# Kernel tuning notes

Measured on AMD Instinct MI355X. Metric: run time of the kernel, lower is better.

The kernel has to match this reference:

```python
import jax, jax.numpy as jnp
import numpy as np

WINDOW = 64
BAND_NUM = 2 * WINDOW      # 128
FILTER_LEN = 6 * WINDOW    # 384


def setup_inputs() -> dict:
    key = jax.random.key(0)
    k1, k2 = jax.random.split(key)
    B, C, T, F = 16, 1, 8192, WINDOW + 1  # F = band_num/2 + 1 = 65
    inp = jax.random.normal(k1, (B, C, T, F), dtype=jnp.float32)
    subband_filter = jax.random.normal(k2, (FILTER_LEN,), dtype=jnp.float32)
    lengths = jnp.full((B,), T, dtype=jnp.int32)  # one sample per batch element, all length T
    return {"input": inp, "subband_filter": subband_filter, "lengths": lengths}


def reference(input, subband_filter, lengths):
    B, C, T, F = input.shape
    S = lengths.shape[0]               # sample_num (static)
    x = input.reshape(-1, F)           # (N, F), N = B*C*T
    # torch.fft.irfft(norm='forward') -> jnp.fft.irfft(norm='forward'), out len = 2*(F-1) = band_num
    ifft_out = jnp.fft.irfft(x, norm='forward')          # (N, 128)
    # tile across the 3 band repeats, apply prototype filter and window gain
    wide = jnp.concatenate([ifft_out, ifft_out, ifft_out], axis=1)  # (N, 384)
    wide = wide * subband_filter[None, :] * WINDOW
    N = wide.shape[0]
    H = N // S                          # in_height (= C*T per sample)
    w = wide.reshape(S, H, 6, WINDOW)   # per-sample, per-frame, 6 taps of width `window`
    true_len = H - 5
    # overlap-add: out[s, t] = sum_k w[s, t + 5 - k, k]
    out = w[:, 5:H, 0, :]
    for k in range(1, 6):
        out = out + w[:, 5 - k:H - k, k, :]
    out = out.reshape(B, C, -1)         # (B, C, true_len*window)
    return out / 32768.0
```

## Files before the change

### kernel.cpp

```cpp
#include <hip/hip_runtime.h>
#include <hip/hip_bf16.h>


#define NF 65
#define NT 8192
#define TRUE_LEN 8187
#define FPW 59
#define WPB 139
#define TAB_STRIDE 68
#define YS_STRIDE 66

typedef const __attribute__((address_space(4))) float cfloat;

__device__ float d_tab[33 * TAB_STRIDE];

__global__ void build_tab_kernel() {
    int idx = blockIdx.x * 256 + threadIdx.x;
    if (idx >= 33 * TAB_STRIDE) return;
    int p = idx / TAB_STRIDE, n = idx % TAB_STRIDE;
    if (n >= 65) { d_tab[idx] = 0.0f; return; }
    int m = (n < 33) ? 2 * n : 2 * (n - 33) + 1;
    float w = (m == 0 || m == 64) ? 1.0f : 2.0f;
    int a = (m * p) & 127;
    d_tab[idx] = w * cospif((float)a * (1.0f / 64.0f));
}

__global__ __launch_bounds__(256)
void subband_main_kernel(const float* __restrict__ g_in,
                         const float* __restrict__ g_filt,
                         float* __restrict__ g_out)
{
    __shared__ __hip_bfloat16 Ys[4][64 * YS_STRIDE];

    const int tid  = threadIdx.x;
    const int lane = tid & 63;
    const int wv   = tid >> 6;
    const int wg   = blockIdx.x * 4 + wv;
    const int s     = wg / WPB;
    const int fbase = (wg % WPB) * FPW;
    int h = fbase + lane;
    if (h > NT - 1) h = NT - 1;

    const float* xr = g_in + ((size_t)s * NT + h) * NF;
    float X[NF];
    #pragma unroll
    for (int c = 0; c < 16; ++c) {
        float t4[4];
        __builtin_memcpy(t4, xr + 4 * c, 16);
        X[4 * c + 0] = t4[0]; X[4 * c + 1] = t4[1];
        X[4 * c + 2] = t4[2]; X[4 * c + 3] = t4[3];
    }
    X[64] = xr[64];

    __hip_bfloat16* ys = &Ys[wv][0];
    cfloat* ct = (cfloat*)(unsigned long long)(const float*)d_tab;

    for (int p = 0; p < 33; ++p) {
        cfloat* cf = ct + p * TAB_STRIDE;
        float e0 = 0.0f, e1 = 0.0f, o0 = 0.0f, o1 = 0.0f;
        #pragma unroll
        for (int n = 0; n < 32; n += 2) {
            e0 += cf[n]      * X[2 * n];
            e1 += cf[n + 1]  * X[2 * n + 2];
            o0 += cf[33 + n] * X[2 * n + 1];
            o1 += cf[34 + n] * X[2 * n + 3];
        }
        e0 += cf[32] * X[64];
        const float aE = e0 + e1, aO = o0 + o1;
        ys[lane * YS_STRIDE + p]      = __float2bfloat16(aE + aO);
        ys[lane * YS_STRIDE + 64 - p] = __float2bfloat16(aE - aO);
    }

    const int j = lane;
    float fc[6];
    #pragma unroll
    for (int k = 0; k < 6; ++k) fc[k] = g_filt[k * 64 + j] * (1.0f / 512.0f);
    const int te = j;
    const int to = (j == 0) ? 64 : 64 - j;

    float we[6], wo[6];
    #pragma unroll
    for (int r = 0; r < 5; ++r) {
        we[r] = __bfloat162float(ys[r * YS_STRIDE + te]);
        wo[r] = __bfloat162float(ys[r * YS_STRIDE + to]);
    }
    float* dst = g_out + ((size_t)s * TRUE_LEN + fbase) * 64 + j;

    #pragma unroll
    for (int q = 0; q < FPW; ++q) {
        if (fbase + q >= TRUE_LEN) break;
        we[5] = __bfloat162float(ys[(q + 5) * YS_STRIDE + te]);
        wo[5] = __bfloat162float(ys[(q + 5) * YS_STRIDE + to]);
        const float o = fc[0] * we[5] + fc[1] * wo[4] + fc[2] * we[3]
                      + fc[3] * wo[2] + fc[4] * we[1] + fc[5] * wo[0];
        dst[(size_t)q * 64] = o;
        #pragma unroll
        for (int r = 0; r < 5; ++r) { we[r] = we[r + 1]; wo[r] = wo[r + 1]; }
    }
}

extern "C" void kernel_launch(void* const* d_in, const int* in_sizes, int n_in,
                              void* d_out, int out_size, void* d_ws, size_t ws_size,
                              hipStream_t stream) {
    const float* g_in   = (const float*)d_in[0];
    const float* g_filt = (const float*)d_in[1];
    float* g_out = (float*)d_out;

    build_tab_kernel<<<9, 256, 0, stream>>>();
    subband_main_kernel<<<556, 256, 0, stream>>>(g_in, g_filt, g_out);
}
```

Before: 102.7 us.

## Restructure IDFT as outer-product accumulation with packed bf16x2 shared stores

Transposes the cosine table so the inverse real DFT loops over input bins outer and output bins inner, keeping 66 register accumulators per thread instead of per-output dot products. Outputs are then written to shared memory as packed bf16 pairs in one pass, replacing the scattered 16-bit stores. Launch bounds are raised to request three blocks per CU. The large register-resident accumulator set plus the 65-element input array raises register pressure, which the occupancy hint may force into spills.

```diff
diff --git a/kernel.cpp b/kernel.cpp
--- a/kernel.cpp
+++ b/kernel.cpp
@@ -7,30 +7,29 @@
 #define TRUE_LEN 8187
 #define FPW 59
 #define WPB 139
-#define TAB_STRIDE 68
+#define TABT_STRIDE 36
 #define YS_STRIDE 66
 
 typedef const __attribute__((address_space(4))) float cfloat;
 
-__device__ float d_tab[33 * TAB_STRIDE];
+__device__ float d_tabT[NF * TABT_STRIDE];
 
 __global__ void build_tab_kernel() {
     int idx = blockIdx.x * 256 + threadIdx.x;
-    if (idx >= 33 * TAB_STRIDE) return;
-    int p = idx / TAB_STRIDE, n = idx % TAB_STRIDE;
-    if (n >= 65) { d_tab[idx] = 0.0f; return; }
-    int m = (n < 33) ? 2 * n : 2 * (n - 33) + 1;
+    if (idx >= NF * TABT_STRIDE) return;
+    int m = idx / TABT_STRIDE, p = idx % TABT_STRIDE;
+    if (p >= 33) { d_tabT[idx] = 0.0f; return; }
     float w = (m == 0 || m == 64) ? 1.0f : 2.0f;
     int a = (m * p) & 127;
-    d_tab[idx] = w * cospif((float)a * (1.0f / 64.0f));
+    d_tabT[idx] = w * cospif((float)a * (1.0f / 64.0f));
 }
 
-__global__ __launch_bounds__(256)
+__global__ __launch_bounds__(256, 3)
 void subband_main_kernel(const float* __restrict__ g_in,
                          const float* __restrict__ g_filt,
                          float* __restrict__ g_out)
 {
-    __shared__ __hip_bfloat16 Ys[4][64 * YS_STRIDE];
+    __shared__ __hip_bfloat162 Ys2[4][64 * 33];
 
     const int tid  = threadIdx.x;
     const int lane = tid & 63;
@@ -52,25 +51,35 @@
     }
     X[64] = xr[64];
 
-    __hip_bfloat16* ys = &Ys[wv][0];
-    cfloat* ct = (cfloat*)(unsigned long long)(const float*)d_tab;
+    float E[33], O[33];
+    #pragma unroll
+    for (int p = 0; p < 33; ++p) { E[p] = 0.0f; O[p] = 0.0f; }
 
-    for (int p = 0; p < 33; ++p) {
-        cfloat* cf = ct + p * TAB_STRIDE;
-        float e0 = 0.0f, e1 = 0.0f, o0 = 0.0f, o1 = 0.0f;
+    cfloat* ct = (cfloat*)(unsigned long long)(const float*)d_tabT;
+    #pragma unroll
+    for (int m = 0; m < NF; ++m) {
+        cfloat* c = ct + m * TABT_STRIDE;
+        const float xm = X[m];
+        float* acc = (m & 1) ? O : E;
         #pragma unroll
-        for (int n = 0; n < 32; n += 2) {
-            e0 += cf[n]      * X[2 * n];
-            e1 += cf[n + 1]  * X[2 * n + 2];
-            o0 += cf[33 + n] * X[2 * n + 1];
-            o1 += cf[34 + n] * X[2 * n + 3];
-        }
-        e0 += cf[32] * X[64];
-        const float aE = e0 + e1, aO = o0 + o1;
-        ys[lane * YS_STRIDE + p]      = __float2bfloat16(aE + aO);
-        ys[lane * YS_STRIDE + 64 - p] = __float2bfloat16(aE - aO);
+        for (int p = 0; p < 33; ++p) acc[p] += c[p] * xm;
     }
 
+    __hip_bfloat162* ys2 = &Ys2[wv][0] + lane * 33;
+    #pragma unroll
+    for (int q = 0; q < 33; ++q) {
+        const int t0 = 2 * q, t1 = 2 * q + 1;
+        const float y0 = (t0 <= 32) ? (E[t0] + O[t0]) : (E[64 - t0] - O[64 - t0]);
+        const float y1 = (t1 <= 64)
+                       ? ((t1 <= 32) ? (E[t1] + O[t1]) : (E[64 - t1] - O[64 - t1]))
+                       : 0.0f;
+        __hip_bfloat162 pk;
+        pk.x = __float2bfloat16(y0);
+        pk.y = __float2bfloat16(y1);
+        ys2[q] = pk;
+    }
+
+    const __hip_bfloat16* ys = (const __hip_bfloat16*)&Ys2[wv][0];
     const int j = lane;
     float fc[6];
     #pragma unroll
@@ -106,6 +115,6 @@
     const float* g_filt = (const float*)d_in[1];
     float* g_out = (float*)d_out;
 
-    build_tab_kernel<<<9, 256, 0, stream>>>();
+    build_tab_kernel<<<10, 256, 0, stream>>>();
     subband_main_kernel<<<556, 256, 0, stream>>>(g_in, g_filt, g_out);
 }
```

Result: slower. 108.4 us (+5.6%).
